# Kernel tuning notes

Hardware: AMD Instinct MI355X
Metric: run time of the kernel (lower is better)

Reference implementation:

```python
import jax, jax.numpy as jnp
import numpy as np

N = 100000       # nodes
E = 1600000      # edges
V = 50000        # vocab
H = 256          # embedding dim (hsize)
A = 64           # per-head out dim (asize)
NH = 3           # num_heads
G = 64           # graphs in batch


def setup_inputs() -> dict:
    key = jax.random.key(0)
    ks = jax.random.split(key, 12)
    h0 = jax.random.randint(ks[0], (N,), 0, V)
    src = jax.random.randint(ks[1], (E,), 0, N)
    dst = jax.random.randint(ks[2], (E,), 0, N)
    graph_ids = jnp.sort(jax.random.randint(ks[3], (N,), 0, G))
    s = 0.05
    emb = jax.random.normal(ks[4], (V, H), jnp.float32) * s
    W_fc = jax.random.normal(ks[5], (H, NH * A), jnp.float32) * s   # GATConv fc
    attn_l = jax.random.normal(ks[6], (NH, A), jnp.float32) * s
    attn_r = jax.random.normal(ks[7], (NH, A), jnp.float32) * s
    bias_gat = jax.random.normal(ks[8], (NH, A), jnp.float32) * s
    W1 = jax.random.normal(ks[9], (A, 128), jnp.float32) * s
    b1 = jnp.zeros((128,), jnp.float32)
    W2 = jax.random.normal(ks[10], (128, 16), jnp.float32) * s
    b2 = jnp.zeros((16,), jnp.float32)
    return dict(h0=h0, src=src, dst=dst, graph_ids=graph_ids, emb=emb,
                W_fc=W_fc, attn_l=attn_l, attn_r=attn_r, bias_gat=bias_gat,
                W1=W1, b1=b1, W2=W2, b2=b2)


def reference(h0, src, dst, graph_ids, emb, W_fc, attn_l, attn_r, bias_gat,
              W1, b1, W2, b2):
    # embedding lookup
    h1 = emb[h0]                                            # [N, H]
    # GATConv: linear projection per head
    feat = (h1 @ W_fc).reshape(N, NH, A)                    # [N, NH, A]
    el = jnp.einsum('nha,ha->nh', feat, attn_l)             # [N, NH]
    er = jnp.einsum('nha,ha->nh', feat, attn_r)             # [N, NH]
    e = jax.nn.leaky_relu(el[src] + er[dst], 0.2)           # [E, NH]
    # segment softmax over incoming edges of each dst node
    m = jax.ops.segment_max(e, dst, num_segments=N)         # [N, NH]
    e_exp = jnp.exp(e - m[dst])                             # [E, NH]
    denom = jax.ops.segment_sum(e_exp, dst, num_segments=N) # [N, NH]
    alpha = e_exp / denom[dst]                              # [E, NH]
    # scatter-aggregate messages
    msg = alpha[:, :, None] * feat[src]                     # [E, NH, A]
    rst = jax.ops.segment_sum(msg, dst, num_segments=N)     # [N, NH, A]
    rst = rst + bias_gat[None]                              # GATConv bias
    # relu + mean over heads
    h2 = jnp.mean(jax.nn.relu(rst), axis=1)                 # [N, A]
    # MLP predictor: ReLU then Identity
    h3 = jax.nn.relu(h2 @ W1 + b1) @ W2 + b2                # [N, 16]
    # dgl.mean_nodes: per-graph mean readout
    sums = jax.ops.segment_sum(h3, graph_ids, num_segments=G)            # [G, 16]
    counts = jax.ops.segment_sum(jnp.ones((N,), h3.dtype), graph_ids, num_segments=G)
    return sums / jnp.maximum(counts, 1.0)[:, None]         # [G, 16]
```

## Files before the change

kernel.cpp:

```cpp
#include <hip/hip_runtime.h>
#include <hip/hip_bf16.h>

#define NNODES 100000
#define NEDGES 1600000
#define VOCAB 50000
#define HDIM 256
#define ADIM 64
#define NHEADS 3
#define FDIM 192
#define NGRAPH 64
#define NPART 64

#define CONV_ELEMS (HDIM * FDIM + 128 * 64 + 16 * 128)
#define CONV_BLOCKS ((CONV_ELEMS + 255) / 256)
#define HIST_BLOCKS ((NEDGES + 255) / 256)
#define PROJ_BLOCKS ((VOCAB + 63) / 64)

typedef __attribute__((ext_vector_type(8))) short bf16x8;
typedef __attribute__((ext_vector_type(4))) float f32x4;

__device__ __forceinline__ float bf2f(unsigned short u) {
  return __uint_as_float((unsigned int)u << 16);
}
__device__ __forceinline__ unsigned short f2bf(float f) {
  unsigned int u = __float_as_uint(f);
  u += 0x7FFFu + ((u >> 16) & 1u);
  return (unsigned short)(u >> 16);
}

__global__ __launch_bounds__(256) void conv_hist_kernel(
    const float* __restrict__ Wfc, const float* __restrict__ W1,
    const float* __restrict__ W2, unsigned short* __restrict__ Wt,
    unsigned short* __restrict__ W1t, unsigned short* __restrict__ W2t,
    const int* __restrict__ dst, int* __restrict__ cnt,
    unsigned short* __restrict__ rank16)
{
  if (blockIdx.x < CONV_BLOCKS) {
    int i = blockIdx.x * 256 + threadIdx.x;
    if (i < HDIM * FDIM) {
      int c = i / HDIM, k = i % HDIM;
      Wt[i] = f2bf(Wfc[(size_t)k * FDIM + c]);
    } else if (i < HDIM * FDIM + 128 * 64) {
      int j = i - HDIM * FDIM;
      int c = j / 64, k = j % 64;
      W1t[j] = f2bf(W1[(size_t)k * 128 + c]);
    } else if (i < CONV_ELEMS) {
      int j = i - HDIM * FDIM - 128 * 64;
      int c = j / 128, k = j % 128;
      W2t[j] = f2bf(W2[(size_t)k * 16 + c]);
    }
  } else {
    int e = (blockIdx.x - CONV_BLOCKS) * 256 + threadIdx.x;
    if (e < NEDGES) rank16[e] = (unsigned short)atomicAdd(&cnt[dst[e]], 1);
  }
}

__global__ __launch_bounds__(256) void scan_sum_kernel(
    const int* __restrict__ cnt, int* __restrict__ bsum, int n)
{
  __shared__ int red[256];
  int t = threadIdx.x;
  int base = blockIdx.x * 1024 + t * 4;
  int s = 0;
#pragma unroll
  for (int j = 0; j < 4; ++j) if (base + j < n) s += cnt[base + j];
  red[t] = s;
  __syncthreads();
  for (int o = 128; o > 0; o >>= 1) {
    if (t < o) red[t] += red[t + o];
    __syncthreads();
  }
  if (t == 0) bsum[blockIdx.x] = red[0];
}

__global__ void scan_bsum_kernel(int* bsum, int nb)
{
  if (threadIdx.x == 0 && blockIdx.x == 0) {
    int acc = 0;
    for (int i = 0; i < nb; ++i) { int v = bsum[i]; bsum[i] = acc; acc += v; }
  }
}

__global__ __launch_bounds__(256) void scan_write_kernel(
    const int* __restrict__ cnt, const int* __restrict__ bsum,
    int* __restrict__ offs, int n, int total)
{
  __shared__ int sd[256];
  int t = threadIdx.x;
  int base = blockIdx.x * 1024 + t * 4;
  int c[4];
  int ts = 0;
#pragma unroll
  for (int j = 0; j < 4; ++j) { c[j] = (base + j < n) ? cnt[base + j] : 0; ts += c[j]; }
  sd[t] = ts;
  __syncthreads();
  for (int o = 1; o < 256; o <<= 1) {
    int v = (t >= o) ? sd[t - o] : 0;
    __syncthreads();
    sd[t] += v;
    __syncthreads();
  }
  int run = sd[t] - ts + bsum[blockIdx.x];
#pragma unroll
  for (int j = 0; j < 4; ++j) {
    if (base + j < n) offs[base + j] = run;
    run += c[j];
  }
  if (blockIdx.x == 0 && t == 0) offs[n] = total;
}

__global__ __launch_bounds__(256) void proj_scatter_kernel(
    const float* __restrict__ emb,
    const unsigned short* __restrict__ Wt,
    const float* __restrict__ attn_l, const float* __restrict__ attn_r,
    unsigned short* __restrict__ proj_bf,
    float4* __restrict__ elv4, float4* __restrict__ erv4,
    const int* __restrict__ src, const int* __restrict__ dst,
    const int* __restrict__ h0, const unsigned short* __restrict__ rank16,
    const int* __restrict__ offs, unsigned short* __restrict__ recs16)
{
  if (blockIdx.x >= PROJ_BLOCKS) {
    int e = (blockIdx.x - PROJ_BLOCKS) * 256 + threadIdx.x;
    if (e < NEDGES) {
      int p = offs[dst[e]] + (int)rank16[e];
      recs16[p] = (unsigned short)h0[src[e]];
    }
    return;
  }
  const int wave = threadIdx.x >> 6;
  const int lane = threadIdx.x & 63;
  const int row0 = blockIdx.x * 64 + wave * 16;
  const int cb = lane & 15;
  const int q  = lane >> 4;
  int arow = row0 + cb;
  if (arow >= VOCAB) arow = VOCAB - 1;
  const int kgrp = q * 8;

  f32x4 acc[12];
#pragma unroll
  for (int c = 0; c < 12; ++c) acc[c] = (f32x4){0.f, 0.f, 0.f, 0.f};

  const float* arow_p = &emb[(size_t)arow * HDIM + kgrp];
  const unsigned short* bcol_p = &Wt[(size_t)cb * HDIM + kgrp];

#pragma unroll
  for (int ks = 0; ks < 8; ++ks) {
    float4 f0 = *reinterpret_cast<const float4*>(arow_p + ks * 32);
    float4 f1 = *reinterpret_cast<const float4*>(arow_p + ks * 32 + 4);
    bf16x8 a;
    a[0] = (short)f2bf(f0.x); a[1] = (short)f2bf(f0.y);
    a[2] = (short)f2bf(f0.z); a[3] = (short)f2bf(f0.w);
    a[4] = (short)f2bf(f1.x); a[5] = (short)f2bf(f1.y);
    a[6] = (short)f2bf(f1.z); a[7] = (short)f2bf(f1.w);
#pragma unroll
    for (int c = 0; c < 12; ++c) {
      bf16x8 b = *reinterpret_cast<const bf16x8*>(bcol_p + (size_t)c * 16 * HDIM + ks * 32);
      acc[c] = __builtin_amdgcn_mfma_f32_16x16x32_bf16(a, b, acc[c], 0, 0, 0);
    }
  }

  const int rb = row0 + 4 * q;
#pragma unroll
  for (int i = 0; i < 4; ++i) {
    int r = rb + i;
    if (r < VOCAB) {
#pragma unroll
      for (int c = 0; c < 12; ++c)
        proj_bf[(size_t)r * FDIM + c * 16 + cb] = f2bf(acc[c][i]);
    }
  }

  float al_v[12], ar_v[12];
#pragma unroll
  for (int c = 0; c < 12; ++c) {
    al_v[c] = attn_l[c * 16 + cb];
    ar_v[c] = attn_r[c * 16 + cb];
  }
  float elp[4][3], erp[4][3];
#pragma unroll
  for (int i = 0; i < 4; ++i)
#pragma unroll
    for (int h = 0; h < 3; ++h) {
      float sl = 0.f, sr = 0.f;
#pragma unroll
      for (int cc = 0; cc < 4; ++cc) {
        float v = acc[h * 4 + cc][i];
        sl += v * al_v[h * 4 + cc];
        sr += v * ar_v[h * 4 + cc];
      }
      elp[i][h] = sl; erp[i][h] = sr;
    }
#pragma unroll
  for (int s = 8; s > 0; s >>= 1) {
#pragma unroll
    for (int i = 0; i < 4; ++i)
#pragma unroll
      for (int h = 0; h < 3; ++h) {
        elp[i][h] += __shfl_xor(elp[i][h], s, 64);
        erp[i][h] += __shfl_xor(erp[i][h], s, 64);
      }
  }
  if (cb == 0) {
#pragma unroll
    for (int i = 0; i < 4; ++i) {
      int r = rb + i;
      if (r < VOCAB) {
        elv4[r] = make_float4(elp[i][0], elp[i][1], elp[i][2], 0.f);
        erv4[r] = make_float4(erp[i][0], erp[i][1], erp[i][2], 0.f);
      }
    }
  }
}

__global__ __launch_bounds__(256) void wexp_kernel(
    const unsigned short* __restrict__ recs16, const int* __restrict__ offs,
    const int* __restrict__ h0,
    const float4* __restrict__ elv4, const float4* __restrict__ erv4,
    uint2* __restrict__ wrec, float4* __restrict__ inv4, int N)
{
  int n = blockIdx.x * 256 + threadIdx.x;
  if (n >= N) return;
  const float4 ero = erv4[h0[n]];
  int lo = offs[n], hi = offs[n + 1];
  float d0 = 0.f, d1 = 0.f, d2 = 0.f;
  for (int p = lo; p < hi; ++p) {
    unsigned v = recs16[p];
    float4 ev = elv4[v];
    float e0 = ev.x + ero.x, e1 = ev.y + ero.y, e2 = ev.z + ero.z;
    e0 = e0 > 0.f ? e0 : 0.2f * e0;
    e1 = e1 > 0.f ? e1 : 0.2f * e1;
    e2 = e2 > 0.f ? e2 : 0.2f * e2;
    unsigned short u0 = f2bf(__expf(e0));
    unsigned short u1 = f2bf(__expf(e1));
    unsigned short u2 = f2bf(__expf(e2));
    d0 += bf2f(u0); d1 += bf2f(u1); d2 += bf2f(u2);
    wrec[p] = make_uint2(v | ((unsigned)u0 << 16),
                         (unsigned)u1 | ((unsigned)u2 << 16));
  }
  inv4[n] = make_float4(d0 > 0.f ? 1.f / d0 : 0.f,
                        d1 > 0.f ? 1.f / d1 : 0.f,
                        d2 > 0.f ? 1.f / d2 : 0.f, 0.f);
}

__global__ __launch_bounds__(256) void aggregate_kernel(
    const uint2* __restrict__ wrec, const int* __restrict__ offs,
    const float4* __restrict__ inv4,
    const unsigned short* __restrict__ proj_bf, const float* __restrict__ bias_gat,
    unsigned short* __restrict__ h2bf, int N)
{
  int lane = threadIdx.x & 63;
  int n = blockIdx.x * 4 + (threadIdx.x >> 6);
  if (n >= N) return;
  int lo = offs[n], hi = offs[n + 1];
  float a0 = 0.f, a1 = 0.f, a2 = 0.f;

  int i = lo;
  for (; i + 4 <= hi; i += 4) {
    uint2 r[4];
#pragma unroll
    for (int j = 0; j < 4; ++j) r[j] = wrec[i + j];
    const unsigned short* ps[4];
#pragma unroll
    for (int j = 0; j < 4; ++j)
      ps[j] = &proj_bf[(size_t)(r[j].x & 0xFFFFu) * FDIM];
    float g0[4], g1[4], g2[4];
#pragma unroll
    for (int j = 0; j < 4; ++j) {
      g0[j] = bf2f(ps[j][lane]);
      g1[j] = bf2f(ps[j][64 + lane]);
      g2[j] = bf2f(ps[j][128 + lane]);
    }
#pragma unroll
    for (int j = 0; j < 4; ++j) {
      a0 += bf2f((unsigned short)(r[j].x >> 16)) * g0[j];
      a1 += bf2f((unsigned short)(r[j].y & 0xFFFFu)) * g1[j];
      a2 += bf2f((unsigned short)(r[j].y >> 16)) * g2[j];
    }
  }
  for (; i < hi; ++i) {
    uint2 r = wrec[i];
    const unsigned short* ps = &proj_bf[(size_t)(r.x & 0xFFFFu) * FDIM];
    a0 += bf2f((unsigned short)(r.x >> 16)) * bf2f(ps[lane]);
    a1 += bf2f((unsigned short)(r.y & 0xFFFFu)) * bf2f(ps[64 + lane]);
    a2 += bf2f((unsigned short)(r.y >> 16)) * bf2f(ps[128 + lane]);
  }

  const float4 inv = inv4[n];
  float r0 = a0 * inv.x + bias_gat[lane];
  float r1 = a1 * inv.y + bias_gat[64 + lane];
  float r2 = a2 * inv.z + bias_gat[128 + lane];
  float h2 = (fmaxf(r0, 0.f) + fmaxf(r1, 0.f) + fmaxf(r2, 0.f)) * (1.f / 3.f);
  h2bf[(size_t)n * 64 + lane] = f2bf(h2);
}

__global__ __launch_bounds__(256) void post_mfma_kernel(
    const unsigned short* __restrict__ h2bf,
    const unsigned short* __restrict__ W1t,
    const float* __restrict__ b1,
    const unsigned short* __restrict__ W2t,
    const float* __restrict__ b2, const int* __restrict__ gid,
    float* __restrict__ sums_priv, float* __restrict__ counts_priv, int N)
{
  __shared__ unsigned short z_lds[64 * 128];
  const int wave = threadIdx.x >> 6;
  const int lane = threadIdx.x & 63;
  const int r = lane & 15;
  const int q = lane >> 4;
  const int kg = q * 8;
  const int rw0 = blockIdx.x * 64 + wave * 16;

  int arow = rw0 + r;
  if (arow >= N) arow = N - 1;

  f32x4 acc1[8];
#pragma unroll
  for (int c = 0; c < 8; ++c) acc1[c] = (f32x4){0.f, 0.f, 0.f, 0.f};

#pragma unroll
  for (int ks = 0; ks < 2; ++ks) {
    bf16x8 a = *reinterpret_cast<const bf16x8*>(&h2bf[(size_t)arow * 64 + kg + ks * 32]);
#pragma unroll
    for (int c = 0; c < 8; ++c) {
      bf16x8 b = *reinterpret_cast<const bf16x8*>(&W1t[(size_t)(c * 16 + r) * 64 + kg + ks * 32]);
      acc1[c] = __builtin_amdgcn_mfma_f32_16x16x32_bf16(a, b, acc1[c], 0, 0, 0);
    }
  }
#pragma unroll
  for (int c = 0; c < 8; ++c) {
    float bb = b1[c * 16 + r];
#pragma unroll
    for (int i = 0; i < 4; ++i) {
      float z = acc1[c][i] + bb;
      z = z > 0.f ? z : 0.f;
      z_lds[(wave * 16 + 4 * q + i) * 128 + c * 16 + r] = f2bf(z);
    }
  }
  __syncthreads();

  f32x4 acc2 = (f32x4){0.f, 0.f, 0.f, 0.f};
#pragma unroll
  for (int ks = 0; ks < 4; ++ks) {
    bf16x8 a = *reinterpret_cast<const bf16x8*>(&z_lds[(wave * 16 + r) * 128 + kg + ks * 32]);
    bf16x8 b = *reinterpret_cast<const bf16x8*>(&W2t[(size_t)r * 128 + kg + ks * 32]);
    acc2 = __builtin_amdgcn_mfma_f32_16x16x32_bf16(a, b, acc2, 0, 0, 0);
  }
  const int part = blockIdx.x & (NPART - 1);
  float bb2 = b2[r];
#pragma unroll
  for (int i = 0; i < 4; ++i) {
    int row = rw0 + 4 * q + i;
    if (row < N) {
      int g = gid[row];
      atomicAdd(&sums_priv[(part * NGRAPH + g) * 16 + r], acc2[i] + bb2);
      if (r == 0) atomicAdd(&counts_priv[part * NGRAPH + g], 1.f);
    }
  }
}

__global__ void finalize_kernel(const float* __restrict__ sums_priv,
                                const float* __restrict__ counts_priv,
                                float* __restrict__ out)
{
  int j = threadIdx.x;
  int g = j >> 4;
  float s = 0.f, c = 0.f;
  for (int p = 0; p < NPART; ++p) {
    s += sums_priv[p * NGRAPH * 16 + j];
    c += counts_priv[p * NGRAPH + g];
  }
  out[j] = s / fmaxf(c, 1.f);
}

extern "C" void kernel_launch(void* const* d_in, const int* in_sizes, int n_in,
                              void* d_out, int out_size, void* d_ws, size_t ws_size,
                              hipStream_t stream)
{
  const int*   h0  = (const int*)  d_in[0];
  const int*   src = (const int*)  d_in[1];
  const int*   dst = (const int*)  d_in[2];
  const int*   gid = (const int*)  d_in[3];
  const float* emb = (const float*)d_in[4];
  const float* Wfc = (const float*)d_in[5];
  const float* al  = (const float*)d_in[6];
  const float* ar  = (const float*)d_in[7];
  const float* bg  = (const float*)d_in[8];
  const float* W1  = (const float*)d_in[9];
  const float* b1  = (const float*)d_in[10];
  const float* W2  = (const float*)d_in[11];
  const float* b2  = (const float*)d_in[12];
  float* out = (float*)d_out;

  char* ws = (char*)d_ws;
  size_t off = 0;
  auto alloc = [&](size_t bytes) -> void* {
    off = (off + 255) & ~(size_t)255;
    void* p = ws + off;
    off += bytes;
    return p;
  };
  const size_t CNT_B  = (size_t)NNODES * 4;
  const size_t CNT_BP = (CNT_B + 255) & ~(size_t)255;
  const size_t SUMS_B = (size_t)NPART * NGRAPH * 16 * 4;
  const size_t ZB     = CNT_BP + SUMS_B + (size_t)NPART * NGRAPH * 4;
  char*  zero_base = (char*)alloc(ZB);
  int*   cnt  = (int*)zero_base;
  float* sums = (float*)(zero_base + CNT_BP);
  float* cnts = (float*)(zero_base + CNT_BP + SUMS_B);

  unsigned short* Wt      = (unsigned short*)alloc((size_t)FDIM * HDIM * 2);
  unsigned short* W1t     = (unsigned short*)alloc((size_t)128 * 64 * 2);
  unsigned short* W2t     = (unsigned short*)alloc((size_t)16 * 128 * 2);
  unsigned short* proj_bf = (unsigned short*)alloc((size_t)VOCAB * FDIM * 2);
  unsigned short* h2bf    = (unsigned short*)alloc((size_t)NNODES * 64 * 2);
  unsigned short* recs16  = (unsigned short*)alloc((size_t)NEDGES * 2);
  unsigned short* rank16  = (unsigned short*)alloc((size_t)NEDGES * 2);
  uint2*  wrec   = (uint2*) alloc((size_t)NEDGES * 8);
  float4* elv4   = (float4*)alloc((size_t)VOCAB * 16);
  float4* erv4   = (float4*)alloc((size_t)VOCAB * 16);
  float4* inv4   = (float4*)alloc((size_t)NNODES * 16);
  int*    offs   = (int*)   alloc((size_t)(NNODES + 1) * 4);
  int*    bsum   = (int*)   alloc((size_t)128 * 4);

  hipMemsetAsync(zero_base, 0, ZB, stream);

  const int NB = (NNODES + 1023) / 1024;

  conv_hist_kernel<<<CONV_BLOCKS + HIST_BLOCKS, 256, 0, stream>>>(
      Wfc, W1, W2, Wt, W1t, W2t, dst, cnt, rank16);
  scan_sum_kernel<<<NB, 256, 0, stream>>>(cnt, bsum, NNODES);
  scan_bsum_kernel<<<1, 64, 0, stream>>>(bsum, NB);
  scan_write_kernel<<<NB, 256, 0, stream>>>(cnt, bsum, offs, NNODES, NEDGES);
  proj_scatter_kernel<<<PROJ_BLOCKS + HIST_BLOCKS, 256, 0, stream>>>(
      emb, Wt, al, ar, proj_bf, elv4, erv4,
      src, dst, h0, rank16, offs, recs16);
  wexp_kernel<<<(NNODES + 255) / 256, 256, 0, stream>>>(recs16, offs, h0, elv4, erv4,
                                                        wrec, inv4, NNODES);
  aggregate_kernel<<<(NNODES + 3) / 4, 256, 0, stream>>>(wrec, offs, inv4, proj_bf,
                                                         bg, h2bf, NNODES);
  post_mfma_kernel<<<(NNODES + 63) / 64, 256, 0, stream>>>(h2bf, W1t, b1, W2t, b2, gid,
                                                           sums, cnts, NNODES);
  finalize_kernel<<<1, 1024, 0, stream>>>(sums, cnts, out);
}
```

Measured before the change: 335.4 us.

## Compute edge softmax weights during CSR scatter and fold denominators into aggregation

The per-node wexp pass and the recs16 intermediate array are removed. Each edge's exponentiated attention scores are now computed in an edge-parallel kernel that writes the packed weight record straight into its CSR slot, and the aggregate kernel accumulates the softmax denominators itself. This drops a thread-per-node pass with unbalanced serial loops, the inv4 buffer and one array round trip. In exchange the projection GEMM no longer overlaps with the scatter in one launch, so the scatter must wait for elv4/erv4, and aggregate does a few extra adds per edge.

Result: no change. 340.1 us (+1.4%).

```diff
diff --git a/kernel.cpp b/kernel.cpp
--- a/kernel.cpp
+++ b/kernel.cpp
@@ -14,7 +14,6 @@
 #define CONV_ELEMS (HDIM * FDIM + 128 * 64 + 16 * 128)
 #define CONV_BLOCKS ((CONV_ELEMS + 255) / 256)
 #define HIST_BLOCKS ((NEDGES + 255) / 256)
-#define PROJ_BLOCKS ((VOCAB + 63) / 64)
 
 typedef __attribute__((ext_vector_type(8))) short bf16x8;
 typedef __attribute__((ext_vector_type(4))) float f32x4;
@@ -109,31 +108,20 @@
   if (blockIdx.x == 0 && t == 0) offs[n] = total;
 }
 
-__global__ __launch_bounds__(256) void proj_scatter_kernel(
+__global__ __launch_bounds__(256) void proj_gemm_kernel(
     const float* __restrict__ emb,
     const unsigned short* __restrict__ Wt,
     const float* __restrict__ attn_l, const float* __restrict__ attn_r,
     unsigned short* __restrict__ proj_bf,
-    float4* __restrict__ elv4, float4* __restrict__ erv4,
-    const int* __restrict__ src, const int* __restrict__ dst,
-    const int* __restrict__ h0, const unsigned short* __restrict__ rank16,
-    const int* __restrict__ offs, unsigned short* __restrict__ recs16)
-{
-  if (blockIdx.x >= PROJ_BLOCKS) {
-    int e = (blockIdx.x - PROJ_BLOCKS) * 256 + threadIdx.x;
-    if (e < NEDGES) {
-      int p = offs[dst[e]] + (int)rank16[e];
-      recs16[p] = (unsigned short)h0[src[e]];
-    }
-    return;
-  }
+    float4* __restrict__ elv4, float4* __restrict__ erv4, int V)
+{
   const int wave = threadIdx.x >> 6;
   const int lane = threadIdx.x & 63;
   const int row0 = blockIdx.x * 64 + wave * 16;
   const int cb = lane & 15;
   const int q  = lane >> 4;
   int arow = row0 + cb;
-  if (arow >= VOCAB) arow = VOCAB - 1;
+  if (arow >= V) arow = V - 1;
   const int kgrp = q * 8;
 
   f32x4 acc[12];
@@ -163,7 +151,7 @@
 #pragma unroll
   for (int i = 0; i < 4; ++i) {
     int r = rb + i;
-    if (r < VOCAB) {
+    if (r < V) {
 #pragma unroll
       for (int c = 0; c < 12; ++c)
         proj_bf[(size_t)r * FDIM + c * 16 + cb] = f2bf(acc[c][i]);
@@ -204,7 +192,7 @@
 #pragma unroll
     for (int i = 0; i < 4; ++i) {
       int r = rb + i;
-      if (r < VOCAB) {
+      if (r < V) {
         elv4[r] = make_float4(elp[i][0], elp[i][1], elp[i][2], 0.f);
         erv4[r] = make_float4(erp[i][0], erp[i][1], erp[i][2], 0.f);
       }
@@ -212,39 +200,33 @@
   }
 }
 
-__global__ __launch_bounds__(256) void wexp_kernel(
-    const unsigned short* __restrict__ recs16, const int* __restrict__ offs,
-    const int* __restrict__ h0,
+__global__ __launch_bounds__(256) void scatter_w_kernel(
+    const int* __restrict__ src, const int* __restrict__ dst,
+    const int* __restrict__ h0, const unsigned short* __restrict__ rank16,
+    const int* __restrict__ offs,
     const float4* __restrict__ elv4, const float4* __restrict__ erv4,
-    uint2* __restrict__ wrec, float4* __restrict__ inv4, int N)
-{
-  int n = blockIdx.x * 256 + threadIdx.x;
-  if (n >= N) return;
-  const float4 ero = erv4[h0[n]];
-  int lo = offs[n], hi = offs[n + 1];
-  float d0 = 0.f, d1 = 0.f, d2 = 0.f;
-  for (int p = lo; p < hi; ++p) {
-    unsigned v = recs16[p];
-    float4 ev = elv4[v];
-    float e0 = ev.x + ero.x, e1 = ev.y + ero.y, e2 = ev.z + ero.z;
-    e0 = e0 > 0.f ? e0 : 0.2f * e0;
-    e1 = e1 > 0.f ? e1 : 0.2f * e1;
-    e2 = e2 > 0.f ? e2 : 0.2f * e2;
-    unsigned short u0 = f2bf(__expf(e0));
-    unsigned short u1 = f2bf(__expf(e1));
-    unsigned short u2 = f2bf(__expf(e2));
-    d0 += bf2f(u0); d1 += bf2f(u1); d2 += bf2f(u2);
-    wrec[p] = make_uint2(v | ((unsigned)u0 << 16),
-                         (unsigned)u1 | ((unsigned)u2 << 16));
-  }
-  inv4[n] = make_float4(d0 > 0.f ? 1.f / d0 : 0.f,
-                        d1 > 0.f ? 1.f / d1 : 0.f,
-                        d2 > 0.f ? 1.f / d2 : 0.f, 0.f);
+    uint2* __restrict__ wrec, int E)
+{
+  int e = blockIdx.x * 256 + threadIdx.x;
+  if (e >= E) return;
+  int s = src[e], d = dst[e];
+  unsigned vs = (unsigned)h0[s];
+  float4 el = elv4[vs];
+  float4 er = erv4[(unsigned)h0[d]];
+  float e0 = el.x + er.x, e1 = el.y + er.y, e2 = el.z + er.z;
+  e0 = e0 > 0.f ? e0 : 0.2f * e0;
+  e1 = e1 > 0.f ? e1 : 0.2f * e1;
+  e2 = e2 > 0.f ? e2 : 0.2f * e2;
+  unsigned short u0 = f2bf(__expf(e0));
+  unsigned short u1 = f2bf(__expf(e1));
+  unsigned short u2 = f2bf(__expf(e2));
+  int p = offs[d] + (int)rank16[e];
+  wrec[p] = make_uint2(vs | ((unsigned)u0 << 16),
+                       (unsigned)u1 | ((unsigned)u2 << 16));
 }
 
 __global__ __launch_bounds__(256) void aggregate_kernel(
     const uint2* __restrict__ wrec, const int* __restrict__ offs,
-    const float4* __restrict__ inv4,
     const unsigned short* __restrict__ proj_bf, const float* __restrict__ bias_gat,
     unsigned short* __restrict__ h2bf, int N)
 {
@@ -252,7 +234,7 @@
   int n = blockIdx.x * 4 + (threadIdx.x >> 6);
   if (n >= N) return;
   int lo = offs[n], hi = offs[n + 1];
-  float a0 = 0.f, a1 = 0.f, a2 = 0.f;
+  float a0 = 0.f, a1 = 0.f, a2 = 0.f, d0 = 0.f, d1 = 0.f, d2 = 0.f;
 
   int i = lo;
   for (; i + 4 <= hi; i += 4) {
@@ -272,23 +254,31 @@
     }
 #pragma unroll
     for (int j = 0; j < 4; ++j) {
-      a0 += bf2f((unsigned short)(r[j].x >> 16)) * g0[j];
-      a1 += bf2f((unsigned short)(r[j].y & 0xFFFFu)) * g1[j];
-      a2 += bf2f((unsigned short)(r[j].y >> 16)) * g2[j];
+      float w0 = bf2f((unsigned short)(r[j].x >> 16));
+      float w1 = bf2f((unsigned short)(r[j].y & 0xFFFFu));
+      float w2 = bf2f((unsigned short)(r[j].y >> 16));
+      a0 += w0 * g0[j]; a1 += w1 * g1[j]; a2 += w2 * g2[j];
+      d0 += w0; d1 += w1; d2 += w2;
     }
   }
   for (; i < hi; ++i) {
     uint2 r = wrec[i];
     const unsigned short* ps = &proj_bf[(size_t)(r.x & 0xFFFFu) * FDIM];
-    a0 += bf2f((unsigned short)(r.x >> 16)) * bf2f(ps[lane]);
-    a1 += bf2f((unsigned short)(r.y & 0xFFFFu)) * bf2f(ps[64 + lane]);
-    a2 += bf2f((unsigned short)(r.y >> 16)) * bf2f(ps[128 + lane]);
-  }
-
-  const float4 inv = inv4[n];
-  float r0 = a0 * inv.x + bias_gat[lane];
-  float r1 = a1 * inv.y + bias_gat[64 + lane];
-  float r2 = a2 * inv.z + bias_gat[128 + lane];
+    float w0 = bf2f((unsigned short)(r.x >> 16));
+    float w1 = bf2f((unsigned short)(r.y & 0xFFFFu));
+    float w2 = bf2f((unsigned short)(r.y >> 16));
+    a0 += w0 * bf2f(ps[lane]);
+    a1 += w1 * bf2f(ps[64 + lane]);
+    a2 += w2 * bf2f(ps[128 + lane]);
+    d0 += w0; d1 += w1; d2 += w2;
+  }
+
+  float i0 = d0 > 0.f ? 1.f / d0 : 0.f;
+  float i1 = d1 > 0.f ? 1.f / d1 : 0.f;
+  float i2 = d2 > 0.f ? 1.f / d2 : 0.f;
+  float r0 = a0 * i0 + bias_gat[lane];
+  float r1 = a1 * i1 + bias_gat[64 + lane];
+  float r2 = a2 * i2 + bias_gat[128 + lane];
   float h2 = (fmaxf(r0, 0.f) + fmaxf(r1, 0.f) + fmaxf(r2, 0.f)) * (1.f / 3.f);
   h2bf[(size_t)n * 64 + lane] = f2bf(h2);
 }
@@ -412,12 +402,10 @@
   unsigned short* W2t     = (unsigned short*)alloc((size_t)16 * 128 * 2);
   unsigned short* proj_bf = (unsigned short*)alloc((size_t)VOCAB * FDIM * 2);
   unsigned short* h2bf    = (unsigned short*)alloc((size_t)NNODES * 64 * 2);
-  unsigned short* recs16  = (unsigned short*)alloc((size_t)NEDGES * 2);
   unsigned short* rank16  = (unsigned short*)alloc((size_t)NEDGES * 2);
   uint2*  wrec   = (uint2*) alloc((size_t)NEDGES * 8);
   float4* elv4   = (float4*)alloc((size_t)VOCAB * 16);
   float4* erv4   = (float4*)alloc((size_t)VOCAB * 16);
-  float4* inv4   = (float4*)alloc((size_t)NNODES * 16);
   int*    offs   = (int*)   alloc((size_t)(NNODES + 1) * 4);
   int*    bsum   = (int*)   alloc((size_t)128 * 4);
 
@@ -430,12 +418,11 @@
   scan_sum_kernel<<<NB, 256, 0, stream>>>(cnt, bsum, NNODES);
   scan_bsum_kernel<<<1, 64, 0, stream>>>(bsum, NB);
   scan_write_kernel<<<NB, 256, 0, stream>>>(cnt, bsum, offs, NNODES, NEDGES);
-  proj_scatter_kernel<<<PROJ_BLOCKS + HIST_BLOCKS, 256, 0, stream>>>(
-      emb, Wt, al, ar, proj_bf, elv4, erv4,
-      src, dst, h0, rank16, offs, recs16);
-  wexp_kernel<<<(NNODES + 255) / 256, 256, 0, stream>>>(recs16, offs, h0, elv4, erv4,
-                                                        wrec, inv4, NNODES);
-  aggregate_kernel<<<(NNODES + 3) / 4, 256, 0, stream>>>(wrec, offs, inv4, proj_bf,
+  proj_gemm_kernel<<<(VOCAB + 63) / 64, 256, 0, stream>>>(
+      emb, Wt, al, ar, proj_bf, elv4, erv4, VOCAB);
+  scatter_w_kernel<<<(NEDGES + 255) / 256, 256, 0, stream>>>(
+      src, dst, h0, rank16, offs, elv4, erv4, wrec, NEDGES);
+  aggregate_kernel<<<(NNODES + 3) / 4, 256, 0, stream>>>(wrec, offs, proj_bf,
                                                          bg, h2bf, NNODES);
   post_mfma_kernel<<<(NNODES + 63) / 64, 256, 0, stream>>>(h2bf, W1t, b1, W2t, b2, gid,
                                                            sums, cnts, NNODES);
```
